# Kernel tuning notes

Measured on AMD Instinct MI355X. Metric: run time of the kernel, lower is better.

The kernel has to match this reference:

```python
import jax, jax.numpy as jnp
import numpy as np

NUM_HEADS = 8
B, L, D = 4, 1024, 512


def sinusoidal_embeddings(length, dim, decay_term=10000.0):
    positions = jnp.arange(1 - length, length, dtype=jnp.float32).reshape(-1, 1)
    div_term = jnp.exp(-jnp.arange(0, dim, 2, dtype=jnp.float32) * (np.log(decay_term) / dim))
    return jnp.concatenate([jnp.sin(positions * div_term), jnp.cos(positions * div_term)], axis=1)


def setup_inputs() -> dict:
    key = jax.random.key(0)
    k1, k2 = jax.random.split(key)
    x = jax.random.normal(k1, (B, L, D), dtype=jnp.float32)
    W = jax.random.normal(k2, (D, 3 * D), dtype=jnp.float32) * 0.02
    b = jnp.zeros((3 * D,), dtype=jnp.float32)
    return {"x": x, "W": W, "b": b}


def reference(x, W, b):
    batch, length, dim = x.shape
    d_head = dim // NUM_HEADS
    # pointwise Conv(3*dim, kernel_size=1) == dense projection
    proj = jnp.einsum('bld,de->ble', x, W) + b  # [B, L, 3*dim]
    # split heads exactly as the module: reshape to [B,L,H,3*d_head], move heads, split into q,k,v
    proj = proj.reshape(batch, length, NUM_HEADS, 3 * d_head).transpose(0, 2, 1, 3)
    q, k, v = jnp.split(proj, 3, axis=3)  # each [B, H, L, d_head]
    qk = jnp.einsum('bhqd,bhkd->bhqk', q, k)
    # relative position scores via gather (unoptimized path)
    emb_matrix = sinusoidal_embeddings(length, d_head)  # [2L-1, d_head]
    indices = jnp.arange(length)[:, None] - jnp.arange(length) + length - 1  # [L, L]
    embeddings = emb_matrix[indices]  # [L, L, d_head]
    qe = jnp.einsum('bhqd,qkd->bhqk', q, embeddings)
    weights = jax.nn.softmax((qk + qe) / jnp.sqrt(jnp.float32(d_head)), axis=-1)
    output = jnp.einsum('bhqk,bhkd->bhqd', weights, v)
    return output.transpose(0, 2, 1, 3).reshape(batch, length, dim)
```

## Files before the change

kernel.cpp:

```cpp
#include <hip/hip_runtime.h>

typedef unsigned short UST;
typedef __attribute__((ext_vector_type(8))) __bf16 bf16x8;
typedef __attribute__((ext_vector_type(4))) float f32x4;
typedef __attribute__((ext_vector_type(16))) float f32x16;

#define NB 4
#define NH 8
#define LSEQ 1024
#define DMODEL 512
#define DH 64

__device__ __forceinline__ UST f2bf(float f) {
  union { float f; unsigned u; } v; v.f = f;
  unsigned u = v.u;
  return (UST)((u + 0x7FFFu + ((u >> 16) & 1u)) >> 16);
}
__device__ __forceinline__ float bf2f(UST h) {
  union { unsigned u; float f; } v; v.u = ((unsigned)h) << 16;
  return v.f;
}
__device__ __forceinline__ unsigned cvt_pk_bf16(float lo, float hi) {
  unsigned r;
  asm volatile("v_cvt_pk_bf16_f32 %0, %1, %2" : "=v"(r) : "v"(lo), "v"(hi));
  return r;
}

__global__ void k_convert_x(const float* __restrict__ x, UST* __restrict__ xbf,
                            UST* __restrict__ kext) {
  int bid = blockIdx.x;
  if (bid < 2048) {
    int i = bid * 256 + threadIdx.x;
    float4 v = ((const float4*)x)[i];
    ushort4 o;
    o.x = f2bf(v.x); o.y = f2bf(v.y); o.z = f2bf(v.z); o.w = f2bf(v.w);
    ((ushort4*)xbf)[i] = o;
  } else {
    int gid = (bid - 2048) * 256 + threadIdx.x;
    int j = gid & 31;
    int l = (gid >> 5) & 1023;
    int bh = gid >> 15;
    float dd = exp2f((float)(-2 * j) * 0.20762050593046f);
    float ang = (float)l * dd;
    float s = __sinf(ang), c = __cosf(ang);
    UST* kp = kext + ((size_t)bh * 1024 + l) * 128;
    kp[64 + j] = f2bf(c);
    kp[96 + j] = f2bf(s);
  }
}

__global__ void k_transpose_W(const float* __restrict__ W, UST* __restrict__ WT) {
  __shared__ float tile[64][65];
  int n0 = blockIdx.x * 64;
  int k0 = blockIdx.y * 64;
  int tx = threadIdx.x & 63, ty = threadIdx.x >> 6;
#pragma unroll
  for (int i = 0; i < 16; ++i) {
    int k = ty + i * 4;
    tile[k][tx] = W[(size_t)(k0 + k) * 1536 + n0 + tx];
  }
  __syncthreads();
#pragma unroll
  for (int i = 0; i < 16; ++i) {
    int n = ty + i * 4;
    WT[(size_t)(n0 + n) * 512 + k0 + tx] = f2bf(tile[tx][n]);
  }
}

__global__ __launch_bounds__(256) void k_proj(
    const UST* __restrict__ xbf, const UST* __restrict__ WT, const float* __restrict__ bias,
    UST* __restrict__ qext, UST* __restrict__ kext, UST* __restrict__ vT) {
  int m0 = blockIdx.x * 128;
  int n0 = blockIdx.y * 64;
  int t = threadIdx.x;
  int lane = t & 63, w = t >> 6;
  int wr = w >> 1, wc = w & 1;
  int g = lane >> 4, c16 = lane & 15;

  __shared__ UST AtS[128 * 64];
  __shared__ UST BtS[64 * 64];

  const char* Ag = (const char*)(xbf + (size_t)m0 * 512);
  const char* Bg = (const char*)(WT + (size_t)n0 * 512);

  bf16x8 areg[4], breg[2];
#pragma unroll
  for (int c = 0; c < 4; ++c) {
    int u = c * 256 + t, r = u >> 3, s = u & 7;
    areg[c] = *(const bf16x8*)(Ag + (size_t)r * 1024 + s * 16);
  }
#pragma unroll
  for (int c = 0; c < 2; ++c) {
    int u = c * 256 + t, r = u >> 3, s = u & 7;
    breg[c] = *(const bf16x8*)(Bg + (size_t)r * 1024 + s * 16);
  }

  f32x4 acc[4][2] = {};
  for (int kk = 0; kk < 512; kk += 64) {
    __syncthreads();
#pragma unroll
    for (int c = 0; c < 4; ++c) {
      int u = c * 256 + t, r = u >> 3, s = u & 7;
      *(bf16x8*)((char*)AtS + (size_t)r * 128 + (s ^ (r & 7)) * 16) = areg[c];
    }
#pragma unroll
    for (int c = 0; c < 2; ++c) {
      int u = c * 256 + t, r = u >> 3, s = u & 7;
      *(bf16x8*)((char*)BtS + (size_t)r * 128 + (s ^ (r & 7)) * 16) = breg[c];
    }
    __syncthreads();

    if (kk + 64 < 512) {
      size_t cb = (size_t)(kk + 64) * 2;
#pragma unroll
      for (int c = 0; c < 4; ++c) {
        int u = c * 256 + t, r = u >> 3, s = u & 7;
        areg[c] = *(const bf16x8*)(Ag + (size_t)r * 1024 + cb + s * 16);
      }
#pragma unroll
      for (int c = 0; c < 2; ++c) {
        int u = c * 256 + t, r = u >> 3, s = u & 7;
        breg[c] = *(const bf16x8*)(Bg + (size_t)r * 1024 + cb + s * 16);
      }
    }

#pragma unroll
    for (int kf = 0; kf < 2; ++kf) {
      bf16x8 af[4], bfr[2];
#pragma unroll
      for (int rf = 0; rf < 4; ++rf) {
        int r = wr * 64 + rf * 16 + c16;
        int s = (kf * 4 + g) ^ (r & 7);
        af[rf] = *(const bf16x8*)((const char*)AtS + (size_t)r * 128 + s * 16);
      }
#pragma unroll
      for (int cf = 0; cf < 2; ++cf) {
        int r = wc * 32 + cf * 16 + c16;
        int s = (kf * 4 + g) ^ (r & 7);
        bfr[cf] = *(const bf16x8*)((const char*)BtS + (size_t)r * 128 + s * 16);
      }
      __builtin_amdgcn_s_setprio(1);
#pragma unroll
      for (int rf = 0; rf < 4; ++rf)
#pragma unroll
        for (int cf = 0; cf < 2; ++cf)
          acc[rf][cf] = __builtin_amdgcn_mfma_f32_16x16x32_bf16(af[rf], bfr[cf], acc[rf][cf], 0, 0, 0);
      __builtin_amdgcn_s_setprio(0);
    }
  }

  bool doalpha = (blockIdx.y % 3 == 0);
  if (doalpha) __syncthreads();

#pragma unroll
  for (int rf = 0; rf < 4; ++rf) {
#pragma unroll
    for (int cf = 0; cf < 2; ++cf) {
      int c = n0 + wc * 32 + cf * 16 + c16;
      int h = c / 192, rem = c % 192;
      float bv = bias[c];
#pragma unroll
      for (int r = 0; r < 4; ++r) {
        int row = m0 + wr * 64 + rf * 16 + g * 4 + r;
        int bidx = row >> 10, ltok = row & 1023;
        int bh = bidx * 8 + h;
        float val = acc[rf][cf][r] + bv;
        if (rem < 64) {
          UST qv = f2bf(val * 0.125f);
          qext[((size_t)bh * 1024 + ltok) * 128 + rem] = qv;
          if (doalpha)
            AtS[(size_t)(row - m0) * 64 + rem] = qv;
        } else if (rem < 128)
          kext[((size_t)bh * 1024 + ltok) * 128 + (rem - 64)] = f2bf(val);
        else
          vT[((size_t)bh * 64 + (rem - 128)) * 1024 + ltok] = f2bf(val);
      }
    }
  }

  if (doalpha) {
    __syncthreads();
    int hh = blockIdx.y / 3;
    int rr = t >> 1;
    int row = m0 + rr;
    int bidx = row >> 10, ltok = row & 1023;
    int bh = bidx * 8 + hh;
    UST* qp = qext + ((size_t)bh * 1024 + ltok) * 128;
#pragma unroll
    for (int i = 0; i < 16; ++i) {
      int j = (t & 1) * 16 + i;
      float dd = exp2f((float)(-2 * j) * 0.20762050593046f);
      float ang = (float)ltok * dd;
      float s = __sinf(ang), c = __cosf(ang);
      float qs = bf2f(AtS[(size_t)rr * 64 + j]);
      float qc = bf2f(AtS[(size_t)rr * 64 + 32 + j]);
      qp[64 + j] = f2bf(qs * s + qc * c);
      qp[96 + j] = f2bf(qc * s - qs * c);
    }
  }
}

__global__ __launch_bounds__(256) void k_attn(
    const UST* __restrict__ qext, const UST* __restrict__ kext,
    const UST* __restrict__ vT, float* __restrict__ out) {
  int blk = ((blockIdx.x & 7) << 6) | (blockIdx.x >> 3);
  int qt = blk & 15, bh = blk >> 4;
  int b = bh >> 3, h = bh & 7;
  int q0 = qt * 64;
  int t = threadIdx.x;
  int lane = t & 63, w = t >> 6;
  int l31 = lane & 31, lh = lane >> 5;
  int wq = w >> 1, wk = w & 1;

  __shared__ UST KtS[2][64 * 128];
  __shared__ UST VtS[2][64 * 64];
  __shared__ float Lsum[2][2][32];

  const UST* qbase = qext + ((size_t)bh * 1024 + q0 + wq * 32 + l31) * 128 + lh * 8;
  bf16x8 qf[8];
#pragma unroll
  for (int c = 0; c < 8; ++c) qf[c] = *(const bf16x8*)&qbase[c * 16];

  const char* kgbase = (const char*)(kext + (size_t)bh * 1024 * 128);
  const char* vgbase = (const char*)(vT + (size_t)bh * 64 * 1024);

  f32x16 O[2] = {};
  float l_lane = 0.f;

  bf16x8 kreg[4], vreg[2];
#pragma unroll
  for (int c = 0; c < 4; ++c) {
    int u = c * 256 + t;
    kreg[c] = *(const bf16x8*)(kgbase + (size_t)(u >> 4) * 256 + (u & 15) * 16);
  }
#pragma unroll
  for (int c = 0; c < 2; ++c) {
    int u = c * 256 + t;
    vreg[c] = *(const bf16x8*)(vgbase + (size_t)(u >> 3) * 2048 + (u & 7) * 16);
  }
#pragma unroll
  for (int c = 0; c < 4; ++c) {
    int u = c * 256 + t, r = u >> 4, s = u & 15;
    *(bf16x8*)((char*)KtS[0] + (size_t)r * 256 + (s ^ ((r ^ (r >> 3)) & 7)) * 16) = kreg[c];
  }
#pragma unroll
  for (int c = 0; c < 2; ++c) {
    int u = c * 256 + t, r = u >> 3, s = u & 7;
    *(bf16x8*)((char*)VtS[0] + (size_t)r * 128 + (s ^ ((r ^ (r >> 3)) & 7)) * 16) = vreg[c];
  }
#pragma unroll
  for (int c = 0; c < 4; ++c) {
    int u = c * 256 + t;
    kreg[c] = *(const bf16x8*)(kgbase + 64 * 256 + (size_t)(u >> 4) * 256 + (u & 15) * 16);
  }
#pragma unroll
  for (int c = 0; c < 2; ++c) {
    int u = c * 256 + t;
    vreg[c] = *(const bf16x8*)(vgbase + 64 * 2 + (size_t)(u >> 3) * 2048 + (u & 7) * 16);
  }
  __syncthreads();

  int krow = wk * 32 + l31;
  int ksalt = (krow ^ (krow >> 3)) & 7;

  for (int it = 0; it < 16; ++it) {
    int cur = it & 1;
    const char* Kb = (const char*)(KtS[cur]);
    const char* Vb = (const char*)(VtS[cur]);

    f32x16 sa = {};
#pragma unroll
    for (int kh = 0; kh < 2; ++kh) {
      bf16x8 kfr[4];
#pragma unroll
      for (int kc = 0; kc < 4; ++kc) {
        int slot = ((kh * 4 + kc) * 2 + lh) ^ ksalt;
        kfr[kc] = *(const bf16x8*)(Kb + (size_t)krow * 256 + slot * 16);
      }
      __builtin_amdgcn_s_setprio(1);
#pragma unroll
      for (int kc = 0; kc < 4; ++kc)
        sa = __builtin_amdgcn_mfma_f32_32x32x16_bf16(kfr[kc], qf[kh * 4 + kc], sa, 0, 0, 0);
      __builtin_amdgcn_s_setprio(0);
    }

    float p[16];
#pragma unroll
    for (int i = 0; i < 16; ++i) {
      p[i] = __expf(sa[i]);
      l_lane += p[i];
    }
    unsigned wv[8], xv[8];
#pragma unroll
    for (int j = 0; j < 8; ++j) wv[j] = cvt_pk_bf16(p[2 * j], p[2 * j + 1]);
#pragma unroll
    for (int j = 0; j < 8; ++j) xv[j] = (unsigned)__shfl_xor((int)wv[j], 32, 64);
    int4 pa0i = lh ? (int4){(int)xv[2], (int)xv[3], (int)wv[2], (int)wv[3]}
                   : (int4){(int)wv[0], (int)wv[1], (int)xv[0], (int)xv[1]};
    int4 pa1i = lh ? (int4){(int)xv[6], (int)xv[7], (int)wv[6], (int)wv[7]}
                   : (int4){(int)wv[4], (int)wv[5], (int)xv[4], (int)xv[5]};
    bf16x8 pa[2] = {*(bf16x8*)&pa0i, *(bf16x8*)&pa1i};

#pragma unroll
    for (int dn = 0; dn < 2; ++dn) {
      int d = dn * 32 + l31;
      int dsalt = (d ^ (d >> 3)) & 7;
      bf16x8 vf[2];
#pragma unroll
      for (int kc = 0; kc < 2; ++kc) {
        int slot = (wk * 4 + kc * 2 + lh) ^ dsalt;
        vf[kc] = *(const bf16x8*)(Vb + (size_t)d * 128 + slot * 16);
      }
      __builtin_amdgcn_s_setprio(1);
#pragma unroll
      for (int kc = 0; kc < 2; ++kc)
        O[dn] = __builtin_amdgcn_mfma_f32_32x32x16_bf16(pa[kc], vf[kc], O[dn], 0, 0, 0);
      __builtin_amdgcn_s_setprio(0);
    }

    if (it < 15) {
      char* Kw = (char*)(KtS[cur ^ 1]);
      char* Vw = (char*)(VtS[cur ^ 1]);
#pragma unroll
      for (int c = 0; c < 4; ++c) {
        int u = c * 256 + t, r = u >> 4, s = u & 15;
        *(bf16x8*)(Kw + (size_t)r * 256 + (s ^ ((r ^ (r >> 3)) & 7)) * 16) = kreg[c];
      }
#pragma unroll
      for (int c = 0; c < 2; ++c) {
        int u = c * 256 + t, r = u >> 3, s = u & 7;
        *(bf16x8*)(Vw + (size_t)r * 128 + (s ^ ((r ^ (r >> 3)) & 7)) * 16) = vreg[c];
      }
      if (it < 14) {
        const char* kg = kgbase + (size_t)(it + 2) * 64 * 256;
#pragma unroll
        for (int c = 0; c < 4; ++c) {
          int u = c * 256 + t;
          kreg[c] = *(const bf16x8*)(kg + (size_t)(u >> 4) * 256 + (u & 15) * 16);
        }
        const char* vg = vgbase + (size_t)(it + 2) * 64 * 2;
#pragma unroll
        for (int c = 0; c < 2; ++c) {
          int u = c * 256 + t;
          vreg[c] = *(const bf16x8*)(vg + (size_t)(u >> 3) * 2048 + (u & 7) * 16);
        }
      }
    }
    __syncthreads();
  }

  l_lane += __shfl_xor(l_lane, 32, 64);
  if (lh == 0) Lsum[wk][wq][l31] = l_lane;
  float* scratch = (float*)KtS[0];
  if (wk == 1) {
#pragma unroll
    for (int i = 0; i < 16; ++i) {
      int qr = wq * 32 + ((i & 3) + 8 * (i >> 2) + 4 * lh);
      scratch[qr * 64 + l31] = O[0][i];
      scratch[qr * 64 + 32 + l31] = O[1][i];
    }
  }
  __syncthreads();
  if (wk == 0) {
#pragma unroll
    for (int i = 0; i < 16; ++i) {
      int cr = (i & 3) + 8 * (i >> 2) + 4 * lh;
      int qr = wq * 32 + cr;
      float inv = 1.0f / (Lsum[0][wq][cr] + Lsum[1][wq][cr]);
      float* op = out + ((size_t)b * 1024 + q0 + qr) * 512 + h * 64;
      op[l31] = (O[0][i] + scratch[qr * 64 + l31]) * inv;
      op[32 + l31] = (O[1][i] + scratch[qr * 64 + 32 + l31]) * inv;
    }
  }
}

extern "C" void kernel_launch(void* const* d_in, const int* in_sizes, int n_in,
                              void* d_out, int out_size, void* d_ws, size_t ws_size,
                              hipStream_t stream) {
  const float* x = (const float*)d_in[0];
  const float* W = (const float*)d_in[1];
  const float* bias = (const float*)d_in[2];
  float* out = (float*)d_out;

  UST* ws = (UST*)d_ws;
  UST* xbf  = ws;
  UST* WT   = xbf + 4096 * 512;
  UST* qext = WT + 1536 * 512;
  UST* kext = qext + 32 * 1024 * 128;
  UST* vT   = kext + 32 * 1024 * 128;

  k_convert_x<<<dim3(6144), dim3(256), 0, stream>>>(x, xbf, kext);
  k_transpose_W<<<dim3(24, 8), dim3(256), 0, stream>>>(W, WT);
  k_proj<<<dim3(32, 24), dim3(256), 0, stream>>>(xbf, WT, bias, qext, kext, vT);
  k_attn<<<dim3(512), dim3(256), 0, stream>>>(qext, kext, vT, out);
}
```

Before: 56.61 us.

## Double-buffer projection GEMM LDS tiles and merge setup kernels into one launch

The projection GEMM now keeps two LDS buffers for the A and B tiles. The next tile is written into the other buffer after the MFMAs, so each k-step needs one barrier instead of two, and the global prefetch runs two steps ahead. The x conversion, key position-embedding fill and W transpose kernels are merged into a single launch, removing one launch and one inter-kernel gap. The cost is doubled LDS use in k_proj, which may lower occupancy, and more register pressure from the longer prefetch distance.

```diff
diff --git a/kernel.cpp b/kernel.cpp
--- a/kernel.cpp
+++ b/kernel.cpp
@@ -26,8 +26,10 @@
   return r;
 }
 
-__global__ void k_convert_x(const float* __restrict__ x, UST* __restrict__ xbf,
-                            UST* __restrict__ kext) {
+__global__ void k_setup(const float* __restrict__ x, UST* __restrict__ xbf,
+                        UST* __restrict__ kext,
+                        const float* __restrict__ W, UST* __restrict__ WT) {
+  __shared__ float tile[64][65];
   int bid = blockIdx.x;
   if (bid < 2048) {
     int i = bid * 256 + threadIdx.x;
@@ -35,7 +37,7 @@
     ushort4 o;
     o.x = f2bf(v.x); o.y = f2bf(v.y); o.z = f2bf(v.z); o.w = f2bf(v.w);
     ((ushort4*)xbf)[i] = o;
-  } else {
+  } else if (bid < 6144) {
     int gid = (bid - 2048) * 256 + threadIdx.x;
     int j = gid & 31;
     int l = (gid >> 5) & 1023;
@@ -46,24 +48,22 @@
     UST* kp = kext + ((size_t)bh * 1024 + l) * 128;
     kp[64 + j] = f2bf(c);
     kp[96 + j] = f2bf(s);
-  }
-}
-
-__global__ void k_transpose_W(const float* __restrict__ W, UST* __restrict__ WT) {
-  __shared__ float tile[64][65];
-  int n0 = blockIdx.x * 64;
-  int k0 = blockIdx.y * 64;
-  int tx = threadIdx.x & 63, ty = threadIdx.x >> 6;
-#pragma unroll
-  for (int i = 0; i < 16; ++i) {
-    int k = ty + i * 4;
-    tile[k][tx] = W[(size_t)(k0 + k) * 1536 + n0 + tx];
-  }
-  __syncthreads();
-#pragma unroll
-  for (int i = 0; i < 16; ++i) {
-    int n = ty + i * 4;
-    WT[(size_t)(n0 + n) * 512 + k0 + tx] = f2bf(tile[tx][n]);
+  } else {
+    int tid = bid - 6144;
+    int n0 = (tid % 24) * 64;
+    int k0 = (tid / 24) * 64;
+    int tx = threadIdx.x & 63, ty = threadIdx.x >> 6;
+#pragma unroll
+    for (int i = 0; i < 16; ++i) {
+      int k = ty + i * 4;
+      tile[k][tx] = W[(size_t)(k0 + k) * 1536 + n0 + tx];
+    }
+    __syncthreads();
+#pragma unroll
+    for (int i = 0; i < 16; ++i) {
+      int n = ty + i * 4;
+      WT[(size_t)(n0 + n) * 512 + k0 + tx] = f2bf(tile[tx][n]);
+    }
   }
 }
 
@@ -77,8 +77,8 @@
   int wr = w >> 1, wc = w & 1;
   int g = lane >> 4, c16 = lane & 15;
 
-  __shared__ UST AtS[128 * 64];
-  __shared__ UST BtS[64 * 64];
+  __shared__ UST AtS[2][128 * 64];
+  __shared__ UST BtS[2][64 * 64];
 
   const char* Ag = (const char*)(xbf + (size_t)m0 * 512);
   const char* Bg = (const char*)(WT + (size_t)n0 * 512);
@@ -94,35 +94,33 @@
     int u = c * 256 + t, r = u >> 3, s = u & 7;
     breg[c] = *(const bf16x8*)(Bg + (size_t)r * 1024 + s * 16);
   }
+#pragma unroll
+  for (int c = 0; c < 4; ++c) {
+    int u = c * 256 + t, r = u >> 3, s = u & 7;
+    *(bf16x8*)((char*)AtS[0] + (size_t)r * 128 + (s ^ (r & 7)) * 16) = areg[c];
+  }
+#pragma unroll
+  for (int c = 0; c < 2; ++c) {
+    int u = c * 256 + t, r = u >> 3, s = u & 7;
+    *(bf16x8*)((char*)BtS[0] + (size_t)r * 128 + (s ^ (r & 7)) * 16) = breg[c];
+  }
+#pragma unroll
+  for (int c = 0; c < 4; ++c) {
+    int u = c * 256 + t, r = u >> 3, s = u & 7;
+    areg[c] = *(const bf16x8*)(Ag + (size_t)r * 1024 + 128 + s * 16);
+  }
+#pragma unroll
+  for (int c = 0; c < 2; ++c) {
+    int u = c * 256 + t, r = u >> 3, s = u & 7;
+    breg[c] = *(const bf16x8*)(Bg + (size_t)r * 1024 + 128 + s * 16);
+  }
+  __syncthreads();
 
   f32x4 acc[4][2] = {};
-  for (int kk = 0; kk < 512; kk += 64) {
-    __syncthreads();
-#pragma unroll
-    for (int c = 0; c < 4; ++c) {
-      int u = c * 256 + t, r = u >> 3, s = u & 7;
-      *(bf16x8*)((char*)AtS + (size_t)r * 128 + (s ^ (r & 7)) * 16) = areg[c];
-    }
-#pragma unroll
-    for (int c = 0; c < 2; ++c) {
-      int u = c * 256 + t, r = u >> 3, s = u & 7;
-      *(bf16x8*)((char*)BtS + (size_t)r * 128 + (s ^ (r & 7)) * 16) = breg[c];
-    }
-    __syncthreads();
-
-    if (kk + 64 < 512) {
-      size_t cb = (size_t)(kk + 64) * 2;
-#pragma unroll
-      for (int c = 0; c < 4; ++c) {
-        int u = c * 256 + t, r = u >> 3, s = u & 7;
-        areg[c] = *(const bf16x8*)(Ag + (size_t)r * 1024 + cb + s * 16);
-      }
-#pragma unroll
-      for (int c = 0; c < 2; ++c) {
-        int u = c * 256 + t, r = u >> 3, s = u & 7;
-        breg[c] = *(const bf16x8*)(Bg + (size_t)r * 1024 + cb + s * 16);
-      }
-    }
+  for (int it = 0; it < 8; ++it) {
+    int cur = it & 1;
+    const char* Ab = (const char*)(AtS[cur]);
+    const char* Bb = (const char*)(BtS[cur]);
 
 #pragma unroll
     for (int kf = 0; kf < 2; ++kf) {
@@ -131,13 +129,13 @@
       for (int rf = 0; rf < 4; ++rf) {
         int r = wr * 64 + rf * 16 + c16;
         int s = (kf * 4 + g) ^ (r & 7);
-        af[rf] = *(const bf16x8*)((const char*)AtS + (size_t)r * 128 + s * 16);
+        af[rf] = *(const bf16x8*)(Ab + (size_t)r * 128 + s * 16);
       }
 #pragma unroll
       for (int cf = 0; cf < 2; ++cf) {
         int r = wc * 32 + cf * 16 + c16;
         int s = (kf * 4 + g) ^ (r & 7);
-        bfr[cf] = *(const bf16x8*)((const char*)BtS + (size_t)r * 128 + s * 16);
+        bfr[cf] = *(const bf16x8*)(Bb + (size_t)r * 128 + s * 16);
       }
       __builtin_amdgcn_s_setprio(1);
 #pragma unroll
@@ -147,10 +145,39 @@
           acc[rf][cf] = __builtin_amdgcn_mfma_f32_16x16x32_bf16(af[rf], bfr[cf], acc[rf][cf], 0, 0, 0);
       __builtin_amdgcn_s_setprio(0);
     }
+
+    if (it < 7) {
+      char* Aw = (char*)(AtS[cur ^ 1]);
+      char* Bw = (char*)(BtS[cur ^ 1]);
+#pragma unroll
+      for (int c = 0; c < 4; ++c) {
+        int u = c * 256 + t, r = u >> 3, s = u & 7;
+        *(bf16x8*)(Aw + (size_t)r * 128 + (s ^ (r & 7)) * 16) = areg[c];
+      }
+#pragma unroll
+      for (int c = 0; c < 2; ++c) {
+        int u = c * 256 + t, r = u >> 3, s = u & 7;
+        *(bf16x8*)(Bw + (size_t)r * 128 + (s ^ (r & 7)) * 16) = breg[c];
+      }
+      if (it < 6) {
+        size_t cb = (size_t)(it + 2) * 128;
+#pragma unroll
+        for (int c = 0; c < 4; ++c) {
+          int u = c * 256 + t, r = u >> 3, s = u & 7;
+          areg[c] = *(const bf16x8*)(Ag + (size_t)r * 1024 + cb + s * 16);
+        }
+#pragma unroll
+        for (int c = 0; c < 2; ++c) {
+          int u = c * 256 + t, r = u >> 3, s = u & 7;
+          breg[c] = *(const bf16x8*)(Bg + (size_t)r * 1024 + cb + s * 16);
+        }
+      }
+    }
+    __syncthreads();
   }
 
   bool doalpha = (blockIdx.y % 3 == 0);
-  if (doalpha) __syncthreads();
+  UST* stash = AtS[0];
 
 #pragma unroll
   for (int rf = 0; rf < 4; ++rf) {
@@ -169,7 +196,7 @@
           UST qv = f2bf(val * 0.125f);
           qext[((size_t)bh * 1024 + ltok) * 128 + rem] = qv;
           if (doalpha)
-            AtS[(size_t)(row - m0) * 64 + rem] = qv;
+            stash[(size_t)(row - m0) * 64 + rem] = qv;
         } else if (rem < 128)
           kext[((size_t)bh * 1024 + ltok) * 128 + (rem - 64)] = f2bf(val);
         else
@@ -192,8 +219,8 @@
       float dd = exp2f((float)(-2 * j) * 0.20762050593046f);
       float ang = (float)ltok * dd;
       float s = __sinf(ang), c = __cosf(ang);
-      float qs = bf2f(AtS[(size_t)rr * 64 + j]);
-      float qc = bf2f(AtS[(size_t)rr * 64 + 32 + j]);
+      float qs = bf2f(stash[(size_t)rr * 64 + j]);
+      float qc = bf2f(stash[(size_t)rr * 64 + 32 + j]);
       qp[64 + j] = f2bf(qs * s + qc * c);
       qp[96 + j] = f2bf(qc * s - qs * c);
     }
@@ -389,8 +416,7 @@
   UST* kext = qext + 32 * 1024 * 128;
   UST* vT   = kext + 32 * 1024 * 128;
 
-  k_convert_x<<<dim3(6144), dim3(256), 0, stream>>>(x, xbf, kext);
-  k_transpose_W<<<dim3(24, 8), dim3(256), 0, stream>>>(W, WT);
+  k_setup<<<dim3(6336), dim3(256), 0, stream>>>(x, xbf, kext, W, WT);
   k_proj<<<dim3(32, 24), dim3(256), 0, stream>>>(xbf, WT, bias, qext, kext, vT);
   k_attn<<<dim3(512), dim3(256), 0, stream>>>(qext, kext, vT, out);
 }
```

After: 54.11 us, median of 3. 1.05x faster.
